# Kernel optimization log

Hardware: AMD Instinct MI355X
Metric: run time of the kernel (lower is better)

The kernel has to match this reference:

```python
import jax, jax.numpy as jnp
import numpy as np

B, T, D = 2, 2048, 1024
H, HD = 16, 32
INNER = H * HD
FF = 4 * D
KT, KP = 3, 15


def _layernorm(x, g, b, eps=1e-5):
    mu = jnp.mean(x, axis=-1, keepdims=True)
    var = jnp.var(x, axis=-1, keepdims=True)
    return (x - mu) * jax.lax.rsqrt(var + eps) * g + b


def _causal_dwconv(x, w, b):
    # x: (b,t,d), w: (d,1,k) depthwise kernel; causal left-pad of k-1
    k = w.shape[-1]
    xc = jnp.transpose(x, (0, 2, 1))  # (b,d,t)
    xp = jnp.pad(xc, ((0, 0), (0, 0), (k - 1, 0)))
    y = jax.lax.conv_general_dilated(
        xp, w, window_strides=(1,), padding='VALID',
        feature_group_count=x.shape[-1],
        dimension_numbers=('NCH', 'OIH', 'NCH'))
    return jnp.transpose(y + b[None, :, None], (0, 2, 1))


def _causal_linear_attention(q, k, v, mask):
    # q,k,v: (b,t,h,d); mask: (b,t)
    m = mask[:, :, None, None]
    q = (jax.nn.elu(q) + 1.0) * m
    k = (jax.nn.elu(k) + 1.0) * m
    v = v * m
    kv = jnp.einsum('bthd,bthe->bthde', k, v)
    kv_prefix = jnp.cumsum(kv, axis=1)          # (b,t,h,d,e) large intermediate
    k_prefix = jnp.cumsum(k, axis=1)
    num = jnp.einsum('bthd,bthde->bthe', q, kv_prefix)
    den = jnp.sum(q * k_prefix, axis=-1, keepdims=True)
    return (num / (den + 1e-6)) * m


def setup_inputs() -> dict:
    key = jax.random.key(0)
    ks = jax.random.split(key, 10)
    w = lambda i, shape: jax.random.normal(ks[i], shape, jnp.float32) * 0.02
    return {
        'inputs': jax.random.normal(ks[0], (B, T, D), jnp.float32),
        'mask': jnp.ones((B, T), jnp.float32),
        'ln1_g': jnp.ones((D,), jnp.float32), 'ln1_b': jnp.zeros((D,), jnp.float32),
        'W_in': w(1, (D, D + 3 * INNER)), 'b_in': jnp.zeros((D + 3 * INNER,), jnp.float32),
        'W_c': w(2, (INNER, D)), 'b_c': jnp.zeros((D,), jnp.float32),
        'w_t': w(3, (D, 1, KT)), 'b_t': jnp.zeros((D,), jnp.float32),
        'w_p': w(4, (D, 1, KP)), 'b_p': jnp.zeros((D,), jnp.float32),
        'W_mix': w(5, (3 * D, D)), 'b_mix': jnp.zeros((D,), jnp.float32),
        'ln2_g': jnp.ones((D,), jnp.float32), 'ln2_b': jnp.zeros((D,), jnp.float32),
        'W1': w(6, (D, FF)), 'b1': jnp.zeros((FF,), jnp.float32),
        'W2': w(7, (FF, D)), 'b2': jnp.zeros((D,), jnp.float32),
    }


def reference(inputs, mask, ln1_g, ln1_b, W_in, b_in, W_c, b_c, w_t, b_t,
              w_p, b_p, W_mix, b_mix, ln2_g, ln2_b, W1, b1, W2, b2):
    residual = inputs
    normed = _layernorm(inputs, ln1_g, ln1_b)
    proj = normed @ W_in + b_in
    gate, q, k, v = jnp.split(proj, [D, D + INNER, D + 2 * INNER], axis=-1)
    b, t, _ = inputs.shape
    q = q.reshape(b, t, H, HD)
    k = k.reshape(b, t, H, HD)
    v = v.reshape(b, t, H, HD)
    content = _causal_linear_attention(q, k, v, mask).reshape(b, t, INNER)
    content = content @ W_c + b_c
    temporal = _causal_dwconv(normed, w_t, b_t)
    positional = _causal_dwconv(normed, w_p, b_p)
    mixed = jnp.concatenate((content, temporal, positional), axis=-1) @ W_mix + b_mix
    mask_f = mask[:, :, None]
    out = residual + jax.nn.sigmoid(gate) * mixed  # dropout=0.0 -> identity
    out = out * mask_f
    h = _layernorm(out, ln2_g, ln2_b)
    ffn = jax.nn.gelu(h @ W1 + b1, approximate=False) @ W2 + b2
    out = out + ffn
    return out * mask_f
```

## Files before the change

kernel.cpp:

```cpp
#include <hip/hip_runtime.h>
#include <math.h>

#define BB 2
#define TT 2048
#define DD 1024
#define HH 16
#define INNERD 512
#define FFD 4096
#define NPROJ 2560
#define CATD 3072
#define MROWS (BB*TT)
#define CHUNK 64
#define NCH (TT/CHUNK)
#define BH 32

typedef __bf16 bf16;
typedef __attribute__((ext_vector_type(8))) __bf16 bf16x8;
typedef __attribute__((ext_vector_type(4))) __bf16 bf16x4;
typedef __attribute__((ext_vector_type(4))) float f32x4;

struct Part4 { void* p0; void* p1; void* p2; void* p3; };

__global__ __launch_bounds__(256) void prep_fused(
    const float* __restrict__ inputs, const float* __restrict__ ln1_g,
    const float* __restrict__ ln1_b, bf16* __restrict__ normed,
    const float* __restrict__ W_in,  bf16* __restrict__ wt_in,
    const float* __restrict__ W_c,   bf16* __restrict__ wt_c,
    const float* __restrict__ W_mix, bf16* __restrict__ wt_mix,
    const float* __restrict__ W1,    bf16* __restrict__ wt1,
    const float* __restrict__ W2,    bf16* __restrict__ wt2)
{
    int blk = blockIdx.x, tid = threadIdx.x;
    if (blk < MROWS) {
        int row = blk;
        f32x4 xv = ((const f32x4*)(inputs + (size_t)row * DD))[tid];
        float s = xv[0] + xv[1] + xv[2] + xv[3];
        float s2 = xv[0]*xv[0] + xv[1]*xv[1] + xv[2]*xv[2] + xv[3]*xv[3];
        #pragma unroll
        for (int off = 32; off > 0; off >>= 1) {
            s  += __shfl_xor(s,  off, 64);
            s2 += __shfl_xor(s2, off, 64);
        }
        __shared__ float rs[4], rs2[4];
        int wid = tid >> 6;
        if ((tid & 63) == 0) { rs[wid] = s; rs2[wid] = s2; }
        __syncthreads();
        s  = rs[0] + rs[1] + rs[2] + rs[3];
        s2 = rs2[0] + rs2[1] + rs2[2] + rs2[3];
        float mean = s * (1.0f / DD);
        float var  = s2 * (1.0f / DD) - mean * mean;
        float rstd = rsqrtf(var + 1e-5f);
        f32x4 gv = ((const f32x4*)ln1_g)[tid];
        f32x4 bv = ((const f32x4*)ln1_b)[tid];
        bf16x4 o;
        #pragma unroll
        for (int q = 0; q < 4; q++)
            o[q] = (bf16)((xv[q] - mean) * rstd * gv[q] + bv[q]);
        ((bf16x4*)(normed + (size_t)row * DD))[tid] = o;
        return;
    }
    int tb = blk - MROWS;
    const float* W; bf16* Wt; int Kd, Nd;
    if      (tb < 2560)  {             W = W_in;  Wt = wt_in;  Kd = 1024; Nd = 2560; }
    else if (tb < 3072)  { tb -= 2560; W = W_c;   Wt = wt_c;   Kd = 512;  Nd = 1024; }
    else if (tb < 6144)  { tb -= 3072; W = W_mix; Wt = wt_mix; Kd = 3072; Nd = 1024; }
    else if (tb < 10240) { tb -= 6144; W = W1;    Wt = wt1;    Kd = 1024; Nd = 4096; }
    else                 { tb -= 10240;W = W2;    Wt = wt2;    Kd = 4096; Nd = 1024; }
    int ntx = Nd >> 5;
    int nb = (tb % ntx) * 32, kb = (tb / ntx) * 32;
    __shared__ float t[32][33];
    int tx = tid & 31, ty = tid >> 5;
    #pragma unroll
    for (int r = 0; r < 32; r += 8)
        t[ty + r][tx] = W[(size_t)(kb + ty + r) * Nd + nb + tx];
    __syncthreads();
    #pragma unroll
    for (int r = 0; r < 32; r += 8)
        Wt[(size_t)(nb + ty + r) * Kd + kb + tx] = (bf16)t[tx][ty + r];
}

template<int EPI>
__global__ __launch_bounds__(256, 4) void gemm_mfma(
    const bf16* __restrict__ A,  int lda,
    const bf16* __restrict__ Bt, int ldb,
    const float* __restrict__ bias,
    bf16* __restrict__ Cb, int ldc,
    int K, Part4 part)
{
    __shared__ bf16 As[128 * 64];
    __shared__ bf16 Bs[128 * 64];
    const int tid  = threadIdx.x;
    const int wave = tid >> 6, lane = tid & 63;
    const int m0 = blockIdx.x * 128, n0 = blockIdx.y * 128;
    const int koff = blockIdx.z * K;
    A  += koff;
    Bt += koff;
    const int wr = wave >> 1, wc = wave & 1;
    const int lrow = lane >> 2;
    const int lcol = (lane & 3) * 8;
    const int fm = lane & 15;
    const int fk = (lane >> 4) * 8;

    f32x4 acc[4][4];
    #pragma unroll
    for (int i = 0; i < 4; i++)
        #pragma unroll
        for (int j = 0; j < 4; j++)
            acc[i][j] = (f32x4){0.f, 0.f, 0.f, 0.f};

    for (int k0 = 0; k0 < K; k0 += 64) {
        #pragma unroll
        for (int r = 0; r < 4; r++) {
            int c  = r * 4 + wave;
            int rc = c >> 1, kh = c & 1;
            const bf16* ga = A  + (size_t)(m0 + rc * 16 + lrow) * lda + k0 + kh * 32 + lcol;
            const bf16* gb = Bt + (size_t)(n0 + rc * 16 + lrow) * ldb + k0 + kh * 32 + lcol;
            __builtin_amdgcn_global_load_lds(
                (const __attribute__((address_space(1))) void*)ga,
                (__attribute__((address_space(3))) void*)(As + c * 512), 16, 0, 0);
            __builtin_amdgcn_global_load_lds(
                (const __attribute__((address_space(1))) void*)gb,
                (__attribute__((address_space(3))) void*)(Bs + c * 512), 16, 0, 0);
        }
        __syncthreads();
        #pragma unroll
        for (int ks = 0; ks < 2; ks++) {
            bf16x8 af[4], bfv[4];
            #pragma unroll
            for (int i = 0; i < 4; i++)
                af[i] = *(const bf16x8*)(As + (wr * 4 + i) * 1024 + ks * 512 + fm * 32 + fk);
            #pragma unroll
            for (int j = 0; j < 4; j++)
                bfv[j] = *(const bf16x8*)(Bs + (wc * 4 + j) * 1024 + ks * 512 + fm * 32 + fk);
            #pragma unroll
            for (int i = 0; i < 4; i++)
                #pragma unroll
                for (int j = 0; j < 4; j++)
                    acc[i][j] = __builtin_amdgcn_mfma_f32_16x16x32_bf16(
                        af[i], bfv[j], acc[i][j], 0, 0, 0);
        }
        __syncthreads();
    }

    void* psel = nullptr;
    if constexpr (EPI == 4) {
        int z = blockIdx.z;
        psel = (z == 0) ? part.p0 : (z == 1) ? part.p1 : (z == 2) ? part.p2 : part.p3;
    }

    #pragma unroll
    for (int i = 0; i < 4; i++) {
        int mbase = m0 + wr * 64 + i * 16 + (lane >> 4) * 4;
        #pragma unroll
        for (int j = 0; j < 4; j++) {
            int col = n0 + wc * 64 + j * 16 + (lane & 15);
            float bv = 0.f;
            if constexpr (EPI == 0 || EPI == 1) bv = bias[col];
            #pragma unroll
            for (int r = 0; r < 4; r++) {
                int row = mbase + r;
                float v = acc[i][j][r] + bv;
                if constexpr (EPI == 0) {
                    Cb[(size_t)row * ldc + col] = (bf16)v;
                } else if constexpr (EPI == 1) {
                    float z2 = v * (1.5957691f + 0.07135502f * v * v);
                    v = v / (1.0f + __expf(-z2));
                    Cb[(size_t)row * ldc + col] = (bf16)v;
                } else {
                    ((bf16*)psel)[(size_t)row * DD + col] = (bf16)v;
                }
            }
        }
    }
}

__global__ __launch_bounds__(256) void epi_wc(
    const bf16* __restrict__ P0, const bf16* __restrict__ P1,
    const float* __restrict__ bias, bf16* __restrict__ cat)
{
    int id = blockIdx.x * 256 + threadIdx.x;
    int row = id >> 8, cg = id & 255;
    bf16x4 s0 = ((const bf16x4*)P0)[id];
    bf16x4 s1 = ((const bf16x4*)P1)[id];
    f32x4 b  = ((const f32x4*)bias)[cg];
    bf16x4 o;
    #pragma unroll
    for (int q = 0; q < 4; q++) o[q] = (bf16)((float)s0[q] + (float)s1[q] + b[q]);
    *(bf16x4*)(cat + (size_t)row * CATD + cg * 4) = o;
}

__global__ __launch_bounds__(256) void epi_mix_ln2(
    const bf16* __restrict__ P0, const bf16* __restrict__ P1,
    const bf16* __restrict__ P2, const float* __restrict__ bias,
    const bf16* __restrict__ proj, const float* __restrict__ res,
    const float* __restrict__ mask,
    const float* __restrict__ g2, const float* __restrict__ b2v,
    float* __restrict__ out1, bf16* __restrict__ hbuf)
{
    int row = blockIdx.x, tid = threadIdx.x;
    float m = mask[row];
    size_t off = (size_t)row * DD + tid * 4;
    bf16x4 s0 = *(const bf16x4*)(P0 + off);
    bf16x4 s1 = *(const bf16x4*)(P1 + off);
    bf16x4 s2v = *(const bf16x4*)(P2 + off);
    f32x4 bv = ((const f32x4*)bias)[tid];
    bf16x4 g4 = *(const bf16x4*)(proj + (size_t)row * NPROJ + tid * 4);
    f32x4 rv = ((const f32x4*)(res + (size_t)row * DD))[tid];
    f32x4 v;
    #pragma unroll
    for (int q = 0; q < 4; q++) {
        float sg = 1.0f / (1.0f + __expf(-(float)g4[q]));
        float sv = (float)s0[q] + (float)s1[q] + (float)s2v[q] + bv[q];
        v[q] = (rv[q] + sg * sv) * m;
    }
    ((f32x4*)(out1 + (size_t)row * DD))[tid] = v;
    float s = v[0] + v[1] + v[2] + v[3];
    float s2 = v[0]*v[0] + v[1]*v[1] + v[2]*v[2] + v[3]*v[3];
    #pragma unroll
    for (int off2 = 32; off2 > 0; off2 >>= 1) {
        s  += __shfl_xor(s,  off2, 64);
        s2 += __shfl_xor(s2, off2, 64);
    }
    __shared__ float rs[4], rs2[4];
    int wid = tid >> 6;
    if ((tid & 63) == 0) { rs[wid] = s; rs2[wid] = s2; }
    __syncthreads();
    s  = rs[0] + rs[1] + rs[2] + rs[3];
    s2 = rs2[0] + rs2[1] + rs2[2] + rs2[3];
    float mean = s * (1.0f / DD);
    float var  = s2 * (1.0f / DD) - mean * mean;
    float rstd = rsqrtf(var + 1e-5f);
    f32x4 gg = ((const f32x4*)g2)[tid];
    f32x4 bb = ((const f32x4*)b2v)[tid];
    bf16x4 h;
    #pragma unroll
    for (int q = 0; q < 4; q++)
        h[q] = (bf16)((v[q] - mean) * rstd * gg[q] + bb[q]);
    ((bf16x4*)(hbuf + (size_t)row * DD))[tid] = h;
}

__global__ __launch_bounds__(256) void epi_w2(
    float* __restrict__ d_out, const float* __restrict__ out1,
    const bf16* __restrict__ P0, const bf16* __restrict__ P1,
    const bf16* __restrict__ P2, const bf16* __restrict__ P3,
    const float* __restrict__ bias, const float* __restrict__ mask)
{
    int id = blockIdx.x * 256 + threadIdx.x;
    int row = id >> 8;
    float m = mask[row];
    bf16x4 a0 = ((const bf16x4*)P0)[id];
    bf16x4 a1 = ((const bf16x4*)P1)[id];
    bf16x4 a2 = ((const bf16x4*)P2)[id];
    bf16x4 a3 = ((const bf16x4*)P3)[id];
    f32x4 r = ((const f32x4*)out1)[id];
    f32x4 b = ((const f32x4*)bias)[id & 255];
    f32x4 o;
    #pragma unroll
    for (int q = 0; q < 4; q++) {
        float sv = (float)a0[q] + (float)a1[q] + (float)a2[q] + (float)a3[q];
        o[q] = (r[q] + sv + b[q]) * m;
    }
    ((f32x4*)d_out)[id] = o;
}

__device__ __forceinline__ float phi_f(float x) {
    return x > 0.f ? x + 1.f : __expf(x);
}

__global__ __launch_bounds__(256) void mid_fused(
    const bf16* __restrict__ x,
    const float* __restrict__ w_t, const float* __restrict__ b_t,
    const float* __restrict__ w_p, const float* __restrict__ b_p,
    bf16* __restrict__ cat,
    const bf16* __restrict__ proj, const float* __restrict__ mask,
    float* __restrict__ kvsum, float* __restrict__ kssum)
{
    __shared__ float s_ks[2][CHUNK][32], s_vs[2][CHUNK][32];
    int blk = blockIdx.x, tid = threadIdx.x;
    if (blk < 1024) {
        int id = blk * 256 + tid;
        int cg = id & 127, rp = id >> 7;
        int c0 = cg * 8;
        int row0 = rp * 2;
        int t0 = row0 & (TT - 1);
        bf16x8 xw[16];
        #pragma unroll
        for (int j = 0; j < 16; j++) {
            int t = t0 - 14 + j;
            if (t >= 0)
                xw[j] = *(const bf16x8*)(x + (size_t)(row0 - 14 + j) * DD + c0);
            else
                #pragma unroll
                for (int q = 0; q < 8; q++) xw[j][q] = (bf16)0.f;
        }
        float y15[2][8], y3[2][8];
        #pragma unroll
        for (int q = 0; q < 8; q++) {
            float bp = b_p[c0 + q], bt = b_t[c0 + q];
            y15[0][q] = bp; y15[1][q] = bp;
            y3[0][q] = bt;  y3[1][q] = bt;
        }
        #pragma unroll
        for (int i = 0; i < 15; i++) {
            float wp[8];
            #pragma unroll
            for (int q = 0; q < 8; q++) wp[q] = w_p[(c0 + q) * 15 + i];
            #pragma unroll
            for (int rr = 0; rr < 2; rr++)
                #pragma unroll
                for (int q = 0; q < 8; q++)
                    y15[rr][q] = fmaf(wp[q], (float)xw[rr + i][q], y15[rr][q]);
        }
        #pragma unroll
        for (int i = 0; i < 3; i++) {
            float wt[8];
            #pragma unroll
            for (int q = 0; q < 8; q++) wt[q] = w_t[(c0 + q) * 3 + i];
            #pragma unroll
            for (int rr = 0; rr < 2; rr++)
                #pragma unroll
                for (int q = 0; q < 8; q++)
                    y3[rr][q] = fmaf(wt[q], (float)xw[rr + 12 + i][q], y3[rr][q]);
        }
        #pragma unroll
        for (int rr = 0; rr < 2; rr++) {
            bf16x8 o3, o15;
            #pragma unroll
            for (int q = 0; q < 8; q++) { o3[q] = (bf16)y3[rr][q]; o15[q] = (bf16)y15[rr][q]; }
            *(bf16x8*)(cat + (size_t)(row0 + rr) * CATD + DD + c0)     = o3;
            *(bf16x8*)(cat + (size_t)(row0 + rr) * CATD + 2 * DD + c0) = o15;
        }
        return;
    }
    int w = tid >> 6;
    if (w >= 2) return;
    int lane = tid & 63;
    int ci = (blk - 1024) * 2 + w;
    int c  = ci & (NCH - 1);
    int bh = ci >> 5;
    int b  = bh >> 4, hh = bh & (HH - 1);
    float (*ks)[32] = s_ks[w];
    float (*vs)[32] = s_vs[w];
    int row0 = b * TT + c * CHUNK;
    {
        int row = row0 + lane;
        float m = mask[row];
        const bf16* kp = proj + (size_t)row * NPROJ + DD + INNERD + hh * 32;
        const bf16* vp = kp + INNERD;
        #pragma unroll
        for (int s = 0; s < 4; s++) {
            bf16x8 k8 = *(const bf16x8*)(kp + s * 8);
            bf16x8 v8 = *(const bf16x8*)(vp + s * 8);
            #pragma unroll
            for (int q = 0; q < 8; q++) {
                ks[lane][s * 8 + q] = phi_f((float)k8[q]) * m;
                vs[lane][s * 8 + q] = (float)v8[q] * m;
            }
        }
    }
    int e = lane & 31, d0 = (lane >> 5) * 16;
    float kv[16], ksl[16];
    #pragma unroll
    for (int j = 0; j < 16; j++) { kv[j] = 0.f; ksl[j] = 0.f; }
    for (int t = 0; t < CHUNK; t++) {
        float ve = vs[t][e];
        f32x4 kr[4];
        #pragma unroll
        for (int s = 0; s < 4; s++) kr[s] = *(const f32x4*)&ks[t][d0 + s * 4];
        #pragma unroll
        for (int j = 0; j < 16; j++) {
            float kval = kr[j >> 2][j & 3];
            kv[j] = fmaf(kval, ve, kv[j]);
            ksl[j] += kval;
        }
    }
    size_t base = (size_t)ci * 1024;
    #pragma unroll
    for (int j = 0; j < 16; j++)
        kvsum[base + (size_t)(d0 + j) * 32 + e] = kv[j];
    if (e == 0) {
        #pragma unroll
        for (int j = 0; j < 16; j++)
            kssum[ci * 32 + d0 + j] = ksl[j];
    }
}

__global__ __launch_bounds__(256) void attn_prefix(
    const float* __restrict__ kvsum, const float* __restrict__ kssum,
    float* __restrict__ kvpref, float* __restrict__ kspref)
{
    int bh = blockIdx.x;
    int tid = threadIdx.x;
    float run[4] = {0.f, 0.f, 0.f, 0.f};
    for (int c = 0; c < NCH; c++) {
        size_t base = (size_t)(bh * NCH + c) * 1024 + tid * 4;
        #pragma unroll
        for (int q = 0; q < 4; q++) {
            kvpref[base + q] = run[q];
            run[q] += kvsum[base + q];
        }
    }
    if (tid < 32) {
        float r = 0.f;
        for (int c = 0; c < NCH; c++) {
            kspref[(bh * NCH + c) * 32 + tid] = r;
            r += kssum[(bh * NCH + c) * 32 + tid];
        }
    }
}

__global__ __launch_bounds__(64) void attn_scan(
    const bf16* __restrict__ proj, const float* __restrict__ mask,
    const float* __restrict__ kvpref, const float* __restrict__ kspref,
    bf16* __restrict__ attn_out)
{
    int blk = blockIdx.x;
    int c  = blk & (NCH - 1);
    int bh = blk >> 5;
    int b  = bh >> 4, hh = bh & (HH - 1);
    int lane = threadIdx.x;
    __shared__ float qs[CHUNK][32], ks[CHUNK][32], vs[CHUNK][32];
    __shared__ float ms[CHUNK];
    int row0 = b * TT + c * CHUNK;
    {
        int row = row0 + lane;
        float m = mask[row];
        ms[lane] = m;
        const bf16* qp = proj + (size_t)row * NPROJ + DD + hh * 32;
        const bf16* kp = qp + INNERD;
        const bf16* vp = kp + INNERD;
        #pragma unroll
        for (int s = 0; s < 4; s++) {
            bf16x8 q8 = *(const bf16x8*)(qp + s * 8);
            bf16x8 k8 = *(const bf16x8*)(kp + s * 8);
            bf16x8 v8 = *(const bf16x8*)(vp + s * 8);
            #pragma unroll
            for (int q = 0; q < 8; q++) {
                qs[lane][s * 8 + q] = phi_f((float)q8[q]) * m;
                ks[lane][s * 8 + q] = phi_f((float)k8[q]) * m;
                vs[lane][s * 8 + q] = (float)v8[q] * m;
            }
        }
    }
    int e = lane & 31, d0 = (lane >> 5) * 16;
    float kv[16], ksl[16];
    size_t base = (size_t)blk * 1024;
    #pragma unroll
    for (int j = 0; j < 16; j++) kv[j] = kvpref[base + (size_t)(d0 + j) * 32 + e];
    #pragma unroll
    for (int j = 0; j < 16; j++) ksl[j] = kspref[blk * 32 + d0 + j];
    __syncthreads();
    for (int t = 0; t < CHUNK; t++) {
        float ve = vs[t][e];
        f32x4 kr[4], qr[4];
        #pragma unroll
        for (int s = 0; s < 4; s++) kr[s] = *(const f32x4*)&ks[t][d0 + s * 4];
        #pragma unroll
        for (int s = 0; s < 4; s++) qr[s] = *(const f32x4*)&qs[t][d0 + s * 4];
        float num0 = 0.f, num1 = 0.f, den0 = 0.f, den1 = 0.f;
        #pragma unroll
        for (int j = 0; j < 16; j++) {
            float kval = kr[j >> 2][j & 3], qval = qr[j >> 2][j & 3];
            kv[j]  = fmaf(kval, ve, kv[j]);
            ksl[j] += kval;
            if (j & 1) { num1 = fmaf(qval, kv[j], num1); den1 = fmaf(qval, ksl[j], den1); }
            else       { num0 = fmaf(qval, kv[j], num0); den0 = fmaf(qval, ksl[j], den0); }
        }
        float num = num0 + num1, den = den0 + den1;
        num += __shfl_xor(num, 32, 64);
        den += __shfl_xor(den, 32, 64);
        if (lane < 32)
            attn_out[(size_t)(row0 + t) * INNERD + hh * 32 + e] =
                (bf16)(num / (den + 1e-6f) * ms[t]);
    }
}

extern "C" void kernel_launch(void* const* d_in, const int* in_sizes, int n_in,
                              void* d_out, int out_size, void* d_ws, size_t ws_size,
                              hipStream_t stream)
{
    const float* inputs = (const float*)d_in[0];
    const float* mask   = (const float*)d_in[1];
    const float* ln1_g  = (const float*)d_in[2];
    const float* ln1_b  = (const float*)d_in[3];
    const float* W_in   = (const float*)d_in[4];
    const float* b_in   = (const float*)d_in[5];
    const float* W_c    = (const float*)d_in[6];
    const float* b_c    = (const float*)d_in[7];
    const float* w_t    = (const float*)d_in[8];
    const float* b_t    = (const float*)d_in[9];
    const float* w_p    = (const float*)d_in[10];
    const float* b_p    = (const float*)d_in[11];
    const float* W_mix  = (const float*)d_in[12];
    const float* b_mix  = (const float*)d_in[13];
    const float* ln2_g  = (const float*)d_in[14];
    const float* ln2_b  = (const float*)d_in[15];
    const float* W1     = (const float*)d_in[16];
    const float* b1     = (const float*)d_in[17];
    const float* W2     = (const float*)d_in[18];
    const float* b2     = (const float*)d_in[19];
    float* out = (float*)d_out;

    char* p = (char*)d_ws;
    bf16* normed = (bf16*)p;  p += (size_t)MROWS * DD * 2;
    bf16* proj   = (bf16*)p;  p += (size_t)MROWS * NPROJ * 2;
    bf16* attnb  = (bf16*)p;  p += (size_t)MROWS * INNERD * 2;
    bf16* cat    = (bf16*)p;  p += (size_t)MROWS * CATD * 2;
    float* out1  = (float*)p; p += (size_t)MROWS * DD * 4;
    bf16* hbuf   = (bf16*)p;  p += (size_t)MROWS * DD * 2;
    bf16* wt_in  = (bf16*)p;  p += (size_t)NPROJ * DD * 2;
    bf16* wt_c   = (bf16*)p;  p += (size_t)DD * INNERD * 2;
    bf16* wt_mix = (bf16*)p;  p += (size_t)DD * CATD * 2;
    bf16* wt1    = (bf16*)p;  p += (size_t)FFD * DD * 2;
    bf16* wt2    = (bf16*)p;  p += (size_t)DD * FFD * 2;
    bf16* ffn1   = (bf16*)d_ws;
    float* kvsum = out1;
    float* kvpref= kvsum  + (size_t)BH * NCH * 1024;
    float* kssum = kvpref + (size_t)BH * NCH * 1024;
    float* kspref= kssum  + (size_t)BH * NCH * 32;
    bf16*  c_p0  = (bf16*)d_out;
    bf16*  c_p1  = (bf16*)out1;
    bf16*  m_p0  = (bf16*)d_out;
    bf16*  m_p1  = (bf16*)d_out + (size_t)MROWS * DD;
    bf16*  m_p2  = hbuf;
    bf16*  w2_p0 = cat;
    bf16*  w2_p1 = cat + (size_t)MROWS * DD;
    bf16*  w2_p2 = cat + (size_t)MROWS * DD * 2;
    bf16*  w2_p3 = hbuf;

    prep_fused<<<MROWS + 14336, 256, 0, stream>>>(
        inputs, ln1_g, ln1_b, normed,
        W_in, wt_in, W_c, wt_c, W_mix, wt_mix, W1, wt1, W2, wt2);
    gemm_mfma<0><<<dim3(MROWS/128, NPROJ/128), 256, 0, stream>>>(
        normed, DD, wt_in, DD, b_in, proj, NPROJ, DD, Part4{});
    mid_fused<<<1024 + 512, 256, 0, stream>>>(
        normed, w_t, b_t, w_p, b_p, cat, proj, mask, kvsum, kssum);
    attn_prefix<<<BH, 256, 0, stream>>>(kvsum, kssum, kvpref, kspref);
    attn_scan  <<<BH * NCH, 64, 0, stream>>>(proj, mask, kvpref, kspref, attnb);
    gemm_mfma<4><<<dim3(MROWS/128, DD/128, 2), 256, 0, stream>>>(
        attnb, INNERD, wt_c, INNERD, nullptr, nullptr, DD, INNERD / 2,
        Part4{c_p0, c_p1, nullptr, nullptr});
    epi_wc<<<MROWS * DD / 4 / 256, 256, 0, stream>>>(c_p0, c_p1, b_c, cat);
    gemm_mfma<4><<<dim3(MROWS/128, DD/128, 3), 256, 0, stream>>>(
        cat, CATD, wt_mix, CATD, nullptr, nullptr, DD, CATD / 3,
        Part4{m_p0, m_p1, m_p2, nullptr});
    epi_mix_ln2<<<MROWS, 256, 0, stream>>>(m_p0, m_p1, m_p2, b_mix, proj, inputs,
                                           mask, ln2_g, ln2_b, out1, hbuf);
    gemm_mfma<1><<<dim3(MROWS/128, FFD/128), 256, 0, stream>>>(
        hbuf, DD, wt1, DD, b1, ffn1, FFD, DD, Part4{});
    gemm_mfma<4><<<dim3(MROWS/128, DD/128, 4), 256, 0, stream>>>(
        ffn1, FFD, wt2, FFD, nullptr, nullptr, DD, FFD / 4,
        Part4{w2_p0, w2_p1, w2_p2, w2_p3});
    epi_w2<<<MROWS * DD / 4 / 256, 256, 0, stream>>>(out, out1, w2_p0, w2_p1,
                                                     w2_p2, w2_p3, b2, mask);
}
```

Baseline: 396.3 us.

## Fold chunk prefix into attn_scan and drop split-K for W_c GEMM

Removes the separate attn_prefix kernel: each attn_scan block now sums the chunk kv/k sums of all earlier chunks itself, so the prefix scan happens inside the scan kernel and one launch plus a round trip of prefix buffers go away. In exchange, later chunks read up to 31 previous chunk summaries, which adds redundant global reads. Separately, the W_c projection GEMM no longer splits K in two with partial outputs and an epi_wc reduction kernel. It runs as a single GEMM with a bias epilogue writing straight into cat, which removes a launch and the partial-sum traffic but leaves the GEMM with fewer blocks.

After: 409.2 us. 3.2% more time.

```diff
diff --git a/kernel.cpp b/kernel.cpp
--- a/kernel.cpp
+++ b/kernel.cpp
@@ -172,21 +172,6 @@
             }
         }
     }
-}
-
-__global__ __launch_bounds__(256) void epi_wc(
-    const bf16* __restrict__ P0, const bf16* __restrict__ P1,
-    const float* __restrict__ bias, bf16* __restrict__ cat)
-{
-    int id = blockIdx.x * 256 + threadIdx.x;
-    int row = id >> 8, cg = id & 255;
-    bf16x4 s0 = ((const bf16x4*)P0)[id];
-    bf16x4 s1 = ((const bf16x4*)P1)[id];
-    f32x4 b  = ((const f32x4*)bias)[cg];
-    bf16x4 o;
-    #pragma unroll
-    for (int q = 0; q < 4; q++) o[q] = (bf16)((float)s0[q] + (float)s1[q] + b[q]);
-    *(bf16x4*)(cat + (size_t)row * CATD + cg * 4) = o;
 }
 
 __global__ __launch_bounds__(256) void epi_mix_ln2(
@@ -385,33 +370,9 @@
     }
 }
 
-__global__ __launch_bounds__(256) void attn_prefix(
-    const float* __restrict__ kvsum, const float* __restrict__ kssum,
-    float* __restrict__ kvpref, float* __restrict__ kspref)
-{
-    int bh = blockIdx.x;
-    int tid = threadIdx.x;
-    float run[4] = {0.f, 0.f, 0.f, 0.f};
-    for (int c = 0; c < NCH; c++) {
-        size_t base = (size_t)(bh * NCH + c) * 1024 + tid * 4;
-        #pragma unroll
-        for (int q = 0; q < 4; q++) {
-            kvpref[base + q] = run[q];
-            run[q] += kvsum[base + q];
-        }
-    }
-    if (tid < 32) {
-        float r = 0.f;
-        for (int c = 0; c < NCH; c++) {
-            kspref[(bh * NCH + c) * 32 + tid] = r;
-            r += kssum[(bh * NCH + c) * 32 + tid];
-        }
-    }
-}
-
 __global__ __launch_bounds__(64) void attn_scan(
     const bf16* __restrict__ proj, const float* __restrict__ mask,
-    const float* __restrict__ kvpref, const float* __restrict__ kspref,
+    const float* __restrict__ kvsum, const float* __restrict__ kssum,
     bf16* __restrict__ attn_out)
 {
     int blk = blockIdx.x;
@@ -444,11 +405,17 @@
     }
     int e = lane & 31, d0 = (lane >> 5) * 16;
     float kv[16], ksl[16];
-    size_t base = (size_t)blk * 1024;
-    #pragma unroll
-    for (int j = 0; j < 16; j++) kv[j] = kvpref[base + (size_t)(d0 + j) * 32 + e];
-    #pragma unroll
-    for (int j = 0; j < 16; j++) ksl[j] = kspref[blk * 32 + d0 + j];
+    #pragma unroll
+    for (int j = 0; j < 16; j++) { kv[j] = 0.f; ksl[j] = 0.f; }
+    for (int cp = 0; cp < c; cp++) {
+        size_t cb = (size_t)(bh * NCH + cp) * 1024;
+        #pragma unroll
+        for (int j = 0; j < 16; j++)
+            kv[j] += kvsum[cb + (size_t)(d0 + j) * 32 + e];
+        #pragma unroll
+        for (int j = 0; j < 16; j++)
+            ksl[j] += kssum[(bh * NCH + cp) * 32 + d0 + j];
+    }
     __syncthreads();
     for (int t = 0; t < CHUNK; t++) {
         float ve = vs[t][e];
@@ -515,11 +482,7 @@
     bf16* wt2    = (bf16*)p;  p += (size_t)DD * FFD * 2;
     bf16* ffn1   = (bf16*)d_ws;
     float* kvsum = out1;
-    float* kvpref= kvsum  + (size_t)BH * NCH * 1024;
-    float* kssum = kvpref + (size_t)BH * NCH * 1024;
-    float* kspref= kssum  + (size_t)BH * NCH * 32;
-    bf16*  c_p0  = (bf16*)d_out;
-    bf16*  c_p1  = (bf16*)out1;
+    float* kssum = kvsum + (size_t)BH * NCH * 1024;
     bf16*  m_p0  = (bf16*)d_out;
     bf16*  m_p1  = (bf16*)d_out + (size_t)MROWS * DD;
     bf16*  m_p2  = hbuf;
@@ -535,12 +498,9 @@
         normed, DD, wt_in, DD, b_in, proj, NPROJ, DD, Part4{});
     mid_fused<<<1024 + 512, 256, 0, stream>>>(
         normed, w_t, b_t, w_p, b_p, cat, proj, mask, kvsum, kssum);
-    attn_prefix<<<BH, 256, 0, stream>>>(kvsum, kssum, kvpref, kspref);
-    attn_scan  <<<BH * NCH, 64, 0, stream>>>(proj, mask, kvpref, kspref, attnb);
-    gemm_mfma<4><<<dim3(MROWS/128, DD/128, 2), 256, 0, stream>>>(
-        attnb, INNERD, wt_c, INNERD, nullptr, nullptr, DD, INNERD / 2,
-        Part4{c_p0, c_p1, nullptr, nullptr});
-    epi_wc<<<MROWS * DD / 4 / 256, 256, 0, stream>>>(c_p0, c_p1, b_c, cat);
+    attn_scan<<<BH * NCH, 64, 0, stream>>>(proj, mask, kvsum, kssum, attnb);
+    gemm_mfma<0><<<dim3(MROWS/128, DD/128), 256, 0, stream>>>(
+        attnb, INNERD, wt_c, INNERD, b_c, cat, CATD, INNERD, Part4{});
     gemm_mfma<4><<<dim3(MROWS/128, DD/128, 3), 256, 0, stream>>>(
         cat, CATD, wt_mix, CATD, nullptr, nullptr, DD, CATD / 3,
         Part4{m_p0, m_p1, m_p2, nullptr});
```
